# Kernel optimization log

Hardware: AMD Instinct MI355X
Metric: run time of the kernel (lower is better)

The kernel has to match this reference:

```python
import jax, jax.numpy as jnp
import numpy as np

B, F, V, D_EMB = 16384, 32, 50000, 16
D_IN = F * D_EMB            # 512, concat embedding dim
N_TASK, N_SPEC, N_SH = 2, 2, 2
E = N_TASK * N_SPEC + N_SH  # 6 experts per CGC level
H1, H2 = 512, 256           # expert_params dims
T1, T2 = 128, 64            # tower dims


def setup_inputs() -> dict:
    key = jax.random.key(0)
    ks = iter(jax.random.split(key, 32))
    def w(shape, s=0.05):
        return jax.random.normal(next(ks), shape, jnp.float32) * s
    return dict(
        x_ids=jax.random.randint(next(ks), (B, F), 0, V),
        emb=w((F, V, D_EMB)),
        e1_W1=w((E, D_IN, H1)), e1_b1=jnp.zeros((E, H1), jnp.float32),
        e1_W2=w((E, H1, H2)), e1_b2=jnp.zeros((E, H2), jnp.float32),
        g1_Ws=w((N_TASK, D_IN, N_SPEC + N_SH)), g1_bs=jnp.zeros((N_TASK, N_SPEC + N_SH), jnp.float32),
        g1_Wsh=w((D_IN, E)), g1_bsh=jnp.zeros((E,), jnp.float32),
        e2_W1=w((E, H2, H1)), e2_b1=jnp.zeros((E, H1), jnp.float32),
        e2_W2=w((E, H1, H2)), e2_b2=jnp.zeros((E, H2), jnp.float32),
        g2_Ws=w((N_TASK, H2, N_SPEC + N_SH)), g2_bs=jnp.zeros((N_TASK, N_SPEC + N_SH), jnp.float32),
        tw_W1=w((N_TASK, H2, T1)), tw_b1=jnp.zeros((N_TASK, T1), jnp.float32),
        tw_W2=w((N_TASK, T1, T2)), tw_b2=jnp.zeros((N_TASK, T2), jnp.float32),
    )


def _cgc(x_list, W1, b1, W2, b2, Wg, bg, Wg_sh=None, bg_sh=None):
    # Stack expert inputs: task-t specific experts read x_list[t], shared read x_list[-1].
    X = jnp.stack([x_list[0]] * N_SPEC + [x_list[1]] * N_SPEC + [x_list[-1]] * N_SH)  # [E,B,Din]
    # Grouped two-layer expert MLP (BatchNorm is identity at eval-mode init).
    h = jax.nn.relu(jnp.einsum('ebd,edh->ebh', X, W1) + b1[:, None, :])   # [E,B,H1]
    out = jax.nn.relu(jnp.einsum('ebh,eho->ebo', h, W2) + b2[:, None, :])  # [E,B,H2]
    outs = []
    for t in range(N_TASK):
        gate = jax.nn.softmax(x_list[t] @ Wg[t] + bg[t], axis=-1)          # [B, N_SPEC+N_SH]
        sel = jnp.concatenate([out[t * N_SPEC:(t + 1) * N_SPEC], out[-N_SH:]], axis=0)
        outs.append(jnp.einsum('bk,kbo->bo', gate, sel))
    if Wg_sh is not None:  # shared gate only for levels < n_level
        gate = jax.nn.softmax(x_list[-1] @ Wg_sh + bg_sh, axis=-1)          # [B,E]
        outs.append(jnp.einsum('bk,kbo->bo', gate, out))
    return outs


def reference(x_ids, emb, e1_W1, e1_b1, e1_W2, e1_b2, g1_Ws, g1_bs, g1_Wsh, g1_bsh,
              e2_W1, e2_b1, e2_W2, e2_b2, g2_Ws, g2_bs, tw_W1, tw_b1, tw_W2, tw_b2):
    # Embedding lookup per sparse feature, then flatten (squeeze_dim=True).
    embed_x = emb[jnp.arange(F)[None, :], x_ids].reshape(B, D_IN)  # [B, 512]
    xs = [embed_x] * (N_TASK + 1)
    xs = _cgc(xs, e1_W1, e1_b1, e1_W2, e1_b2, g1_Ws, g1_bs, g1_Wsh, g1_bsh)  # level 1 -> 3 outs
    xs = _cgc(xs, e2_W1, e2_b1, e2_W2, e2_b2, g2_Ws, g2_bs)                  # level 2 -> 2 outs
    ys = []
    for t in range(N_TASK):
        h = jax.nn.relu(xs[t] @ tw_W1[t] + tw_b1[t])
        h = jax.nn.relu(h @ tw_W2[t] + tw_b2[t])
        ys.append(jax.nn.sigmoid(h))  # PredictionLayer('classification')
    return jnp.concatenate(ys, axis=1)  # [B, N_TASK*T2]
```

## Files before the change

kernel.cpp:

```cpp
#include <hip/hip_runtime.h>

typedef unsigned short u16;
typedef __attribute__((ext_vector_type(4))) unsigned short u16x4;
typedef __attribute__((ext_vector_type(8))) unsigned short u16x8;
typedef __attribute__((ext_vector_type(8))) short s16x8;
typedef __attribute__((ext_vector_type(4))) float f32x4;

#define BATCH 16384
#define NFEAT 32
#define NVOCAB 50000

__device__ __forceinline__ u16 f2bf(float f) {
    union { float f; unsigned u; } v; v.f = f;
    unsigned u = v.u;
    return (u16)((u + 0x7fffu + ((u >> 16) & 1u)) >> 16);
}
__device__ __forceinline__ float bf2f(u16 h) {
    union { unsigned u; float f; } v; v.u = ((unsigned)h) << 16;
    return v.f;
}

__device__ __forceinline__ void load_lds16(const u16* g, u16* l) {
    __builtin_amdgcn_global_load_lds(
        (const __attribute__((address_space(1))) void*)g,
        (__attribute__((address_space(3))) void*)l, 16, 0, 0);
}

struct PrepDesc { const float* src; u16* dst; int K; int N; int nz; int zbase; };
struct PrepArgs { PrepDesc d[6]; };

__global__ void prep_weights(PrepArgs args) {
    int z = blockIdx.z;
    int di = 0;
    #pragma unroll
    for (int i = 0; i < 6; i++)
        if (z >= args.d[i].zbase && z < args.d[i].zbase + args.d[i].nz) di = i;
    PrepDesc d = args.d[di];
    int zz = z - d.zbase;
    int k0 = blockIdx.x * 32, n0 = blockIdx.y * 32;
    if (k0 >= d.K || n0 >= d.N) return;
    __shared__ float tile[32][33];
    const float* src = d.src + (long)zz * d.K * d.N;
    u16* dst = d.dst + (long)zz * d.K * d.N;
    int tx = threadIdx.x & 31, ty = threadIdx.x >> 5;
    for (int r = ty; r < 32; r += 8) {
        int k = k0 + r, n = n0 + tx;
        tile[r][tx] = (k < d.K && n < d.N) ? src[(long)k * d.N + n] : 0.f;
    }
    __syncthreads();
    for (int r = ty; r < 32; r += 8) {
        int n = n0 + r, k = k0 + tx;
        if (n < d.N && k < d.K) dst[(long)n * d.K + k] = f2bf(tile[tx][r]);
    }
}

__global__ void gather_embed(const int* __restrict__ ids,
                             const float* __restrict__ emb,
                             u16* __restrict__ out) {
    int idx = blockIdx.x * 256 + threadIdx.x;
    int d4 = idx & 3;
    int f  = (idx >> 2) & 31;
    int b  = idx >> 7;
    int id = ids[b * NFEAT + f];
    const float4* p = (const float4*)(emb + ((long)f * NVOCAB + id) * 16) + d4;
    float4 v = *p;
    u16x4 o;
    o.x = f2bf(v.x); o.y = f2bf(v.y); o.z = f2bf(v.z); o.w = f2bf(v.w);
    *(u16x4*)(out + (long)b * 512 + f * 16 + d4 * 4) = o;
}

struct GemmP {
    const u16* A; const u16* Bt; const float* bias; u16* C;
    int N, K, a_zshift, c_row_stride; long a_zstride, c_zstride;
};

__device__ __forceinline__ void gemm_impl(const GemmP p) {
    __shared__ u16 sA[128 * 64];
    __shared__ u16 sB[256 * 64];
    const int z = blockIdx.z;
    const u16* Ab = p.A + (long)(z >> p.a_zshift) * p.a_zstride;
    const u16* Bb = p.Bt + (long)z * p.N * p.K;
    const int m0 = blockIdx.x * 128;
    const int n0 = blockIdx.y * 256;
    const int tid = threadIdx.x;
    const int lane = tid & 63;
    const int w = tid >> 6;
    const int wm = (w & 1) * 64;
    const int wn = (w >> 1) * 128;
    const int l16 = lane & 15;
    const int q = lane >> 4;
    const int key = l16 & 7;
    const int K = p.K;

    const int tr = tid >> 3;
    const int lc = (tid & 7) ^ (tr & 7);
    const u16* gA0 = Ab + (long)(m0 + tr) * K + lc * 8;
    const u16* gB0 = Bb + (long)(n0 + tr) * K + lc * 8;
    u16* lA0 = &sA[(tid & ~63) * 8];
    u16* lB0 = &sB[(tid & ~63) * 8];

    f32x4 acc[4][8] = {};

    for (int k0 = 0; k0 < K; k0 += 64) {
        if (k0) __syncthreads();
        #pragma unroll
        for (int i = 0; i < 4; i++)
            load_lds16(gA0 + (long)(32 * i) * K + k0, lA0 + i * 256 * 8);
        #pragma unroll
        for (int i = 0; i < 8; i++)
            load_lds16(gB0 + (long)(32 * i) * K + k0, lB0 + i * 256 * 8);
        __syncthreads();
        #pragma unroll
        for (int kk = 0; kk < 2; kk++) {
            const int pc = ((kk << 2) | q) ^ key;
            s16x8 af[4], bf[8];
            #pragma unroll
            for (int mt = 0; mt < 4; mt++)
                af[mt] = *(const s16x8*)(&sA[(wm + mt * 16 + l16) * 64 + pc * 8]);
            #pragma unroll
            for (int nt = 0; nt < 8; nt++)
                bf[nt] = *(const s16x8*)(&sB[(wn + nt * 16 + l16) * 64 + pc * 8]);
            #pragma unroll
            for (int mt = 0; mt < 4; mt++)
                #pragma unroll
                for (int nt = 0; nt < 8; nt++)
                    acc[mt][nt] = __builtin_amdgcn_mfma_f32_16x16x32_bf16(
                        bf[nt], af[mt], acc[mt][nt], 0, 0, 0);
        }
    }

    const float* bb = p.bias + (long)z * p.N;
    u16* Cp = p.C + (long)z * p.c_zstride;
    #pragma unroll
    for (int mt = 0; mt < 4; mt++) {
        int grow = m0 + wm + mt * 16 + l16;
        u16* rowp = Cp + (long)grow * p.c_row_stride;
        #pragma unroll
        for (int nt = 0; nt < 8; nt++) {
            int gc = n0 + wn + nt * 16 + q * 4;
            float4 bv = *(const float4*)(bb + gc);
            f32x4 v = acc[mt][nt];
            v.x = fmaxf(v.x + bv.x, 0.f);
            v.y = fmaxf(v.y + bv.y, 0.f);
            v.z = fmaxf(v.z + bv.z, 0.f);
            v.w = fmaxf(v.w + bv.w, 0.f);
            u16x4 o;
            o.x = f2bf(v.x); o.y = f2bf(v.y); o.z = f2bf(v.z); o.w = f2bf(v.w);
            *(u16x4*)(rowp + gc) = o;
        }
    }
}

__global__ __launch_bounds__(256, 2) void gemm_l1a(GemmP p) { gemm_impl(p); }
__global__ __launch_bounds__(256, 2) void gemm_l1b(GemmP p) { gemm_impl(p); }
__global__ __launch_bounds__(256, 2) void gemm_l2a(GemmP p) { gemm_impl(p); }
__global__ __launch_bounds__(256, 2) void gemm_l2b(GemmP p) { gemm_impl(p); }

__global__ __launch_bounds__(256, 1)
void tower_fused(const u16* __restrict__ x2, const u16* __restrict__ W1t,
                 const float* __restrict__ b1, const u16* __restrict__ W2t,
                 const float* __restrict__ b2, float* __restrict__ out) {
    const int t = blockIdx.y, m0 = blockIdx.x * 64;
    __shared__ u16 sX[64 * 256];
    __shared__ u16 sW1[128 * 256];
    __shared__ u16 sH[64 * 136];
    __shared__ u16 sW2[64 * 128];
    __shared__ float sB1[128];
    __shared__ float sB2[64];
    const int tid = threadIdx.x, lane = tid & 63, w = tid >> 6;
    const int l16 = lane & 15, q = lane >> 4;

    #pragma unroll
    for (int i = 0; i < 8; i++) {
        int c = i * 256 + tid, row = c >> 5, kc = c & 31;
        int lcc = (kc & ~7) | ((kc & 7) ^ (row & 7));
        load_lds16(x2 + ((long)t * BATCH + m0 + row) * 256 + lcc * 8,
                   &sX[(i * 256 + (tid & ~63)) * 8]);
    }
    #pragma unroll
    for (int i = 0; i < 16; i++) {
        int c = i * 256 + tid, row = c >> 5, kc = c & 31;
        int lcc = (kc & ~7) | ((kc & 7) ^ (row & 7));
        load_lds16(W1t + ((long)t * 128 + row) * 256 + lcc * 8,
                   &sW1[(i * 256 + (tid & ~63)) * 8]);
    }
    #pragma unroll
    for (int i = 0; i < 4; i++) {
        int c = i * 256 + tid, row = c >> 4, kc = c & 15;
        int lcc = (kc & ~7) | ((kc & 7) ^ (row & 7));
        load_lds16(W2t + ((long)t * 64 + row) * 128 + lcc * 8,
                   &sW2[(i * 256 + (tid & ~63)) * 8]);
    }
    if (tid < 128) sB1[tid] = b1[t * 128 + tid];
    if (tid < 64)  sB2[tid] = b2[t * 64 + tid];
    __syncthreads();

    f32x4 acc1[4][2] = {};
    #pragma unroll
    for (int kk = 0; kk < 8; kk++) {
        int pcb = kk * 4 + q;
        s16x8 af[4], bf[2];
        #pragma unroll
        for (int mt = 0; mt < 4; mt++) {
            int row = mt * 16 + l16;
            int sc = (pcb & ~7) | ((pcb & 7) ^ (row & 7));
            af[mt] = *(const s16x8*)(&sX[row * 256 + sc * 8]);
        }
        #pragma unroll
        for (int nt = 0; nt < 2; nt++) {
            int row = w * 32 + nt * 16 + l16;
            int sc = (pcb & ~7) | ((pcb & 7) ^ (row & 7));
            bf[nt] = *(const s16x8*)(&sW1[row * 256 + sc * 8]);
        }
        #pragma unroll
        for (int mt = 0; mt < 4; mt++)
            #pragma unroll
            for (int nt = 0; nt < 2; nt++)
                acc1[mt][nt] = __builtin_amdgcn_mfma_f32_16x16x32_bf16(
                    bf[nt], af[mt], acc1[mt][nt], 0, 0, 0);
    }
    #pragma unroll
    for (int mt = 0; mt < 4; mt++) {
        int row = mt * 16 + l16;
        #pragma unroll
        for (int nt = 0; nt < 2; nt++) {
            int col = w * 32 + nt * 16 + q * 4;
            f32x4 v = acc1[mt][nt];
            u16x4 o;
            o.x = f2bf(fmaxf(v.x + sB1[col + 0], 0.f));
            o.y = f2bf(fmaxf(v.y + sB1[col + 1], 0.f));
            o.z = f2bf(fmaxf(v.z + sB1[col + 2], 0.f));
            o.w = f2bf(fmaxf(v.w + sB1[col + 3], 0.f));
            *(u16x4*)(&sH[row * 136 + col]) = o;
        }
    }
    __syncthreads();

    f32x4 acc2[4] = {};
    #pragma unroll
    for (int kk = 0; kk < 4; kk++) {
        s16x8 af[4], bf;
        #pragma unroll
        for (int mt = 0; mt < 4; mt++) {
            int row = mt * 16 + l16;
            af[mt] = *(const s16x8*)(&sH[row * 136 + kk * 32 + q * 8]);
        }
        {
            int row = w * 16 + l16;
            int pc = kk * 4 + q;
            int sc = (pc & ~7) | ((pc & 7) ^ (row & 7));
            bf = *(const s16x8*)(&sW2[row * 128 + sc * 8]);
        }
        #pragma unroll
        for (int mt = 0; mt < 4; mt++)
            acc2[mt] = __builtin_amdgcn_mfma_f32_16x16x32_bf16(
                bf, af[mt], acc2[mt], 0, 0, 0);
    }
    #pragma unroll
    for (int mt = 0; mt < 4; mt++) {
        int grow = m0 + mt * 16 + l16;
        int col = w * 16 + q * 4;
        float4 bv = *(const float4*)(sB2 + col);
        f32x4 v = acc2[mt];
        float4 r;
        r.x = 1.f / (1.f + __expf(-(v.x + bv.x)));
        r.y = 1.f / (1.f + __expf(-(v.y + bv.y)));
        r.z = 1.f / (1.f + __expf(-(v.z + bv.z)));
        r.w = 1.f / (1.f + __expf(-(v.w + bv.w)));
        *(float4*)(out + (long)grow * 128 + t * 64 + col) = r;
    }
}

__global__ __launch_bounds__(256)
void gate1(const u16* __restrict__ embed, const u16* __restrict__ out1,
           const float* __restrict__ g1Ws, const float* __restrict__ g1bs,
           const float* __restrict__ gWsh, const float* __restrict__ gbsh,
           u16* __restrict__ x1) {
    const int m0 = blockIdx.x * 8;
    __shared__ float sg[8][16];
    const int tid = threadIdx.x;
    const int row = tid >> 5, l = tid & 31;
    const long rb = m0 + row;

    float a[4] = {0,0,0,0}, b[4] = {0,0,0,0}, c[6] = {0,0,0,0,0,0};
    {
        const u16* er = embed + rb * 512 + l * 16;
        u16x8 xa = *(const u16x8*)(er);
        u16x8 xb = *(const u16x8*)(er + 8);
        #pragma unroll
        for (int u = 0; u < 16; u++) {
            int k = l * 16 + u;
            float xv = bf2f(u < 8 ? xa[u] : xb[u - 8]);
            float4 wa = *(const float4*)(g1Ws + k * 4);
            float4 wb = *(const float4*)(g1Ws + 2048 + k * 4);
            a[0] += xv * wa.x; a[1] += xv * wa.y; a[2] += xv * wa.z; a[3] += xv * wa.w;
            b[0] += xv * wb.x; b[1] += xv * wb.y; b[2] += xv * wb.z; b[3] += xv * wb.w;
            float2 w0 = *(const float2*)(gWsh + k * 6);
            float2 w1 = *(const float2*)(gWsh + k * 6 + 2);
            float2 w2 = *(const float2*)(gWsh + k * 6 + 4);
            c[0] += xv * w0.x; c[1] += xv * w0.y;
            c[2] += xv * w1.x; c[3] += xv * w1.y;
            c[4] += xv * w2.x; c[5] += xv * w2.y;
        }
    }
    #pragma unroll
    for (int off = 1; off < 32; off <<= 1) {
        #pragma unroll
        for (int g = 0; g < 4; g++) { a[g] += __shfl_xor(a[g], off); b[g] += __shfl_xor(b[g], off); }
        #pragma unroll
        for (int g = 0; g < 6; g++) c[g] += __shfl_xor(c[g], off);
    }
    if (l == 0) {
        float mx, s, e[6];
        mx = -1e30f;
        for (int g = 0; g < 4; g++) { a[g] += g1bs[g]; mx = fmaxf(mx, a[g]); }
        s = 0.f; for (int g = 0; g < 4; g++) { e[g] = __expf(a[g] - mx); s += e[g]; }
        for (int g = 0; g < 4; g++) sg[row][g] = e[g] / s;
        mx = -1e30f;
        for (int g = 0; g < 4; g++) { b[g] += g1bs[4 + g]; mx = fmaxf(mx, b[g]); }
        s = 0.f; for (int g = 0; g < 4; g++) { e[g] = __expf(b[g] - mx); s += e[g]; }
        for (int g = 0; g < 4; g++) sg[row][4 + g] = e[g] / s;
        mx = -1e30f;
        for (int g = 0; g < 6; g++) { c[g] += gbsh[g]; mx = fmaxf(mx, c[g]); }
        s = 0.f; for (int g = 0; g < 6; g++) { e[g] = __expf(c[g] - mx); s += e[g]; }
        for (int g = 0; g < 6; g++) sg[row][8 + g] = e[g] / s;
    }
    __syncthreads();

    const int c8 = l * 8;
    const u16* ob = out1 + rb * 256 + c8;
    u16x8 o[6];
    #pragma unroll
    for (int k = 0; k < 6; k++) o[k] = *(const u16x8*)(ob + (long)k * BATCH * 256);
    const float* g = sg[row];
    u16x8 r0, r1, r2;
    #pragma unroll
    for (int u = 0; u < 8; u++) {
        float o0 = bf2f(o[0][u]), o1 = bf2f(o[1][u]), o2 = bf2f(o[2][u]);
        float o3 = bf2f(o[3][u]), o4 = bf2f(o[4][u]), o5 = bf2f(o[5][u]);
        r0[u] = f2bf(g[0] * o0 + g[1] * o1 + g[2] * o4 + g[3] * o5);
        r1[u] = f2bf(g[4] * o2 + g[5] * o3 + g[6] * o4 + g[7] * o5);
        r2[u] = f2bf(g[8] * o0 + g[9] * o1 + g[10] * o2 + g[11] * o3 + g[12] * o4 + g[13] * o5);
    }
    *(u16x8*)(x1 + ((long)0 * BATCH + rb) * 256 + c8) = r0;
    *(u16x8*)(x1 + ((long)1 * BATCH + rb) * 256 + c8) = r1;
    *(u16x8*)(x1 + ((long)2 * BATCH + rb) * 256 + c8) = r2;
}

__global__ __launch_bounds__(256)
void gate2(const u16* __restrict__ x1, const u16* __restrict__ out2,
           const float* __restrict__ g2Ws, const float* __restrict__ g2bs,
           u16* __restrict__ x2) {
    const int m0 = blockIdx.x * 8;
    __shared__ float sg[8][8];
    const int tid = threadIdx.x;
    const int row = tid >> 5, l = tid & 31;
    const long rb = m0 + row;

    float a[4] = {0,0,0,0}, b[4] = {0,0,0,0};
    {
        const u16* e0 = x1 + rb * 256 + l * 8;
        const u16* e1 = e0 + (long)BATCH * 256;
        u16x8 x0 = *(const u16x8*)e0;
        u16x8 x1v = *(const u16x8*)e1;
        #pragma unroll
        for (int u = 0; u < 8; u++) {
            int k = l * 8 + u;
            float4 wa = *(const float4*)(g2Ws + k * 4);
            float4 wb = *(const float4*)(g2Ws + 1024 + k * 4);
            float xv0 = bf2f(x0[u]), xv1 = bf2f(x1v[u]);
            a[0] += xv0 * wa.x; a[1] += xv0 * wa.y; a[2] += xv0 * wa.z; a[3] += xv0 * wa.w;
            b[0] += xv1 * wb.x; b[1] += xv1 * wb.y; b[2] += xv1 * wb.z; b[3] += xv1 * wb.w;
        }
    }
    #pragma unroll
    for (int off = 1; off < 32; off <<= 1) {
        #pragma unroll
        for (int g = 0; g < 4; g++) { a[g] += __shfl_xor(a[g], off); b[g] += __shfl_xor(b[g], off); }
    }
    if (l == 0) {
        float mx, s, e[4];
        mx = -1e30f;
        for (int g = 0; g < 4; g++) { a[g] += g2bs[g]; mx = fmaxf(mx, a[g]); }
        s = 0.f; for (int g = 0; g < 4; g++) { e[g] = __expf(a[g] - mx); s += e[g]; }
        for (int g = 0; g < 4; g++) sg[row][g] = e[g] / s;
        mx = -1e30f;
        for (int g = 0; g < 4; g++) { b[g] += g2bs[4 + g]; mx = fmaxf(mx, b[g]); }
        s = 0.f; for (int g = 0; g < 4; g++) { e[g] = __expf(b[g] - mx); s += e[g]; }
        for (int g = 0; g < 4; g++) sg[row][4 + g] = e[g] / s;
    }
    __syncthreads();

    const int c8 = l * 8;
    const u16* ob = out2 + rb * 256 + c8;
    u16x8 o[6];
    #pragma unroll
    for (int k = 0; k < 6; k++) o[k] = *(const u16x8*)(ob + (long)k * BATCH * 256);
    const float* g = sg[row];
    u16x8 r0, r1;
    #pragma unroll
    for (int u = 0; u < 8; u++) {
        float o0 = bf2f(o[0][u]), o1 = bf2f(o[1][u]), o2 = bf2f(o[2][u]);
        float o3 = bf2f(o[3][u]), o4 = bf2f(o[4][u]), o5 = bf2f(o[5][u]);
        r0[u] = f2bf(g[0] * o0 + g[1] * o1 + g[2] * o4 + g[3] * o5);
        r1[u] = f2bf(g[4] * o2 + g[5] * o3 + g[6] * o4 + g[7] * o5);
    }
    *(u16x8*)(x2 + ((long)0 * BATCH + rb) * 256 + c8) = r0;
    *(u16x8*)(x2 + ((long)1 * BATCH + rb) * 256 + c8) = r1;
}

extern "C" void kernel_launch(void* const* d_in, const int* in_sizes, int n_in,
                              void* d_out, int out_size, void* d_ws, size_t ws_size,
                              hipStream_t stream) {
    const int*   x_ids = (const int*)  d_in[0];
    const float* emb   = (const float*)d_in[1];
    const float* e1W1  = (const float*)d_in[2];
    const float* e1b1  = (const float*)d_in[3];
    const float* e1W2  = (const float*)d_in[4];
    const float* e1b2  = (const float*)d_in[5];
    const float* g1Ws  = (const float*)d_in[6];
    const float* g1bs  = (const float*)d_in[7];
    const float* g1Wsh = (const float*)d_in[8];
    const float* g1bsh = (const float*)d_in[9];
    const float* e2W1  = (const float*)d_in[10];
    const float* e2b1  = (const float*)d_in[11];
    const float* e2W2  = (const float*)d_in[12];
    const float* e2b2  = (const float*)d_in[13];
    const float* g2Ws  = (const float*)d_in[14];
    const float* g2bs  = (const float*)d_in[15];
    const float* twW1  = (const float*)d_in[16];
    const float* twb1  = (const float*)d_in[17];
    const float* twW2  = (const float*)d_in[18];
    const float* twb2  = (const float*)d_in[19];
    float* out = (float*)d_out;

    char* ws = (char*)d_ws;
    u16* embed   = (u16*)(ws + 0);
    u16* wt_e1W1 = (u16*)(ws + 16777216);
    u16* wt_e1W2 = (u16*)(ws + 19922944);
    u16* wt_e2W1 = (u16*)(ws + 21495808);
    u16* wt_e2W2 = (u16*)(ws + 23068672);
    u16* wt_twW1 = (u16*)(ws + 24641536);
    u16* wt_twW2 = (u16*)(ws + 24772608);
    u16* h_buf   = (u16*)(ws + 24805376);
    u16* o_buf   = (u16*)(ws + 125468672);
    u16* x1      = (u16*)(ws + 175800320);
    u16* x2      = (u16*)(ws + 200966144);

    PrepArgs pa;
    pa.d[0] = { e1W1, wt_e1W1, 512, 512, 6,  0 };
    pa.d[1] = { e1W2, wt_e1W2, 512, 256, 6,  6 };
    pa.d[2] = { e2W1, wt_e2W1, 256, 512, 6, 12 };
    pa.d[3] = { e2W2, wt_e2W2, 512, 256, 6, 18 };
    pa.d[4] = { twW1, wt_twW1, 256, 128, 2, 24 };
    pa.d[5] = { twW2, wt_twW2, 128,  64, 2, 26 };
    prep_weights<<<dim3(16, 16, 28), 256, 0, stream>>>(pa);

    gather_embed<<<dim3(BATCH * NFEAT * 4 / 256), 256, 0, stream>>>(x_ids, emb, embed);

    GemmP p1a = { embed, wt_e1W1, e1b1, h_buf, 512, 512, 0, 512, 0L, (long)BATCH * 512 };
    gemm_l1a<<<dim3(128, 2, 6), 256, 0, stream>>>(p1a);

    GemmP p1b = { h_buf, wt_e1W2, e1b2, o_buf, 256, 512, 0, 256,
                  (long)BATCH * 512, (long)BATCH * 256 };
    gemm_l1b<<<dim3(128, 1, 6), 256, 0, stream>>>(p1b);

    gate1<<<dim3(BATCH / 8), 256, 0, stream>>>(embed, o_buf, g1Ws, g1bs, g1Wsh, g1bsh, x1);

    GemmP p2a = { x1, wt_e2W1, e2b1, h_buf, 512, 256, 1, 512,
                  (long)BATCH * 256, (long)BATCH * 512 };
    gemm_l2a<<<dim3(128, 2, 6), 256, 0, stream>>>(p2a);

    GemmP p2b = { h_buf, wt_e2W2, e2b2, o_buf, 256, 512, 0, 256,
                  (long)BATCH * 512, (long)BATCH * 256 };
    gemm_l2b<<<dim3(128, 1, 6), 256, 0, stream>>>(p2b);

    gate2<<<dim3(BATCH / 8), 256, 0, stream>>>(x1, o_buf, g2Ws, g2bs, x2);

    tower_fused<<<dim3(BATCH / 64, 2), 256, 0, stream>>>(x2, wt_twW1, twb1, wt_twW2, twb2, out);
}
```

Measured before the change: 522.7 us.

## Fuse level-2 gating into tower kernel and merge gather with weight prep

Combines embedding gather and weight transpose/convert into one persistent-style launch. Fuses the level-2 gate softmax and weighted expert mix directly into the tower MLP kernel, so the x2 intermediate is never written to or reread from global memory. Tower weights are now read straight from global/L2 instead of being staged in LDS, which lowers LDS use to allow two blocks per CU. The p1a a_zshift changes from 0 to 3, which only means all experts read the same embed input, the same as before since a_zstride is 0.

```diff
diff --git a/kernel.cpp b/kernel.cpp
--- a/kernel.cpp
+++ b/kernel.cpp
@@ -19,54 +19,65 @@
     union { unsigned u; float f; } v; v.u = ((unsigned)h) << 16;
     return v.f;
 }
-
 __device__ __forceinline__ void load_lds16(const u16* g, u16* l) {
     __builtin_amdgcn_global_load_lds(
         (const __attribute__((address_space(1))) void*)g,
         (__attribute__((address_space(3))) void*)l, 16, 0, 0);
 }
 
-struct PrepDesc { const float* src; u16* dst; int K; int N; int nz; int zbase; };
-struct PrepArgs { PrepDesc d[6]; };
-
-__global__ void prep_weights(PrepArgs args) {
-    int z = blockIdx.z;
-    int di = 0;
-    #pragma unroll
-    for (int i = 0; i < 6; i++)
-        if (z >= args.d[i].zbase && z < args.d[i].zbase + args.d[i].nz) di = i;
-    PrepDesc d = args.d[di];
-    int zz = z - d.zbase;
-    int k0 = blockIdx.x * 32, n0 = blockIdx.y * 32;
-    if (k0 >= d.K || n0 >= d.N) return;
-    __shared__ float tile[32][33];
-    const float* src = d.src + (long)zz * d.K * d.N;
-    u16* dst = d.dst + (long)zz * d.K * d.N;
-    int tx = threadIdx.x & 31, ty = threadIdx.x >> 5;
-    for (int r = ty; r < 32; r += 8) {
-        int k = k0 + r, n = n0 + tx;
-        tile[r][tx] = (k < d.K && n < d.N) ? src[(long)k * d.N + n] : 0.f;
-    }
-    __syncthreads();
-    for (int r = ty; r < 32; r += 8) {
-        int n = n0 + r, k = k0 + tx;
-        if (n < d.N && k < d.K) dst[(long)n * d.K + k] = f2bf(tile[tx][r]);
-    }
-}
-
-__global__ void gather_embed(const int* __restrict__ ids,
-                             const float* __restrict__ emb,
-                             u16* __restrict__ out) {
-    int idx = blockIdx.x * 256 + threadIdx.x;
-    int d4 = idx & 3;
-    int f  = (idx >> 2) & 31;
-    int b  = idx >> 7;
-    int id = ids[b * NFEAT + f];
-    const float4* p = (const float4*)(emb + ((long)f * NVOCAB + id) * 16) + d4;
-    float4 v = *p;
-    u16x4 o;
-    o.x = f2bf(v.x); o.y = f2bf(v.y); o.z = f2bf(v.z); o.w = f2bf(v.w);
-    *(u16x4*)(out + (long)b * 512 + f * 16 + d4 * 4) = o;
+struct P0Args {
+    const int* x_ids; const float* emb;
+    const float* e1W1; const float* e1W2; const float* e2W1; const float* e2W2;
+    const float* twW1; const float* twW2;
+    u16* embed; u16* wt_e1W1; u16* wt_e1W2; u16* wt_e2W1; u16* wt_e2W2;
+    u16* wt_twW1; u16* wt_twW2;
+};
+
+__global__ __launch_bounds__(256)
+void p0_gather_prep(P0Args a) {
+    __shared__ float tile[32 * 33];
+    const int tid = threadIdx.x;
+    if (blockIdx.x < 256) {
+        for (long idx = (long)blockIdx.x * 256 + tid; idx < (long)BATCH * NFEAT * 4;
+             idx += 65536) {
+            int d4 = (int)(idx & 3);
+            int f  = (int)((idx >> 2) & 31);
+            int b  = (int)(idx >> 7);
+            int id = a.x_ids[b * NFEAT + f];
+            float4 v = *((const float4*)(a.emb + ((long)f * NVOCAB + id) * 16) + d4);
+            u16x4 o;
+            o.x = f2bf(v.x); o.y = f2bf(v.y); o.z = f2bf(v.z); o.w = f2bf(v.w);
+            *(u16x4*)(a.embed + (long)b * 512 + f * 16 + d4 * 4) = o;
+        }
+    } else {
+        const int tx = tid & 31, ty = tid >> 5;
+        for (int j = blockIdx.x - 256; j < 7168; j += 256) {
+            int z = j >> 8;
+            int rem = j & 255;
+            const float* src; u16* dst; int K, N, zb;
+            if      (z <  6) { src = a.e1W1; dst = a.wt_e1W1; K = 512; N = 512; zb = 0; }
+            else if (z < 12) { src = a.e1W2; dst = a.wt_e1W2; K = 512; N = 256; zb = 6; }
+            else if (z < 18) { src = a.e2W1; dst = a.wt_e2W1; K = 256; N = 512; zb = 12; }
+            else if (z < 24) { src = a.e2W2; dst = a.wt_e2W2; K = 512; N = 256; zb = 18; }
+            else if (z < 26) { src = a.twW1; dst = a.wt_twW1; K = 256; N = 128; zb = 24; }
+            else             { src = a.twW2; dst = a.wt_twW2; K = 128; N = 64;  zb = 26; }
+            int zz = z - zb;
+            int k0 = (rem & 15) * 32, n0 = (rem >> 4) * 32;
+            if (k0 >= K || n0 >= N) continue;
+            __syncthreads();
+            const float* s = src + (long)zz * K * N;
+            u16* d = dst + (long)zz * K * N;
+            for (int r = ty; r < 32; r += 8) {
+                int k = k0 + r, n = n0 + tx;
+                tile[r * 33 + tx] = (k < K && n < N) ? s[(long)k * N + n] : 0.f;
+            }
+            __syncthreads();
+            for (int r = ty; r < 32; r += 8) {
+                int n = n0 + r, k = k0 + tx;
+                if (n < N && k < K) d[(long)n * K + k] = f2bf(tile[tx * 33 + r]);
+            }
+        }
+    }
 }
 
 struct GemmP {
@@ -156,121 +167,6 @@
 __global__ __launch_bounds__(256, 2) void gemm_l2a(GemmP p) { gemm_impl(p); }
 __global__ __launch_bounds__(256, 2) void gemm_l2b(GemmP p) { gemm_impl(p); }
 
-__global__ __launch_bounds__(256, 1)
-void tower_fused(const u16* __restrict__ x2, const u16* __restrict__ W1t,
-                 const float* __restrict__ b1, const u16* __restrict__ W2t,
-                 const float* __restrict__ b2, float* __restrict__ out) {
-    const int t = blockIdx.y, m0 = blockIdx.x * 64;
-    __shared__ u16 sX[64 * 256];
-    __shared__ u16 sW1[128 * 256];
-    __shared__ u16 sH[64 * 136];
-    __shared__ u16 sW2[64 * 128];
-    __shared__ float sB1[128];
-    __shared__ float sB2[64];
-    const int tid = threadIdx.x, lane = tid & 63, w = tid >> 6;
-    const int l16 = lane & 15, q = lane >> 4;
-
-    #pragma unroll
-    for (int i = 0; i < 8; i++) {
-        int c = i * 256 + tid, row = c >> 5, kc = c & 31;
-        int lcc = (kc & ~7) | ((kc & 7) ^ (row & 7));
-        load_lds16(x2 + ((long)t * BATCH + m0 + row) * 256 + lcc * 8,
-                   &sX[(i * 256 + (tid & ~63)) * 8]);
-    }
-    #pragma unroll
-    for (int i = 0; i < 16; i++) {
-        int c = i * 256 + tid, row = c >> 5, kc = c & 31;
-        int lcc = (kc & ~7) | ((kc & 7) ^ (row & 7));
-        load_lds16(W1t + ((long)t * 128 + row) * 256 + lcc * 8,
-                   &sW1[(i * 256 + (tid & ~63)) * 8]);
-    }
-    #pragma unroll
-    for (int i = 0; i < 4; i++) {
-        int c = i * 256 + tid, row = c >> 4, kc = c & 15;
-        int lcc = (kc & ~7) | ((kc & 7) ^ (row & 7));
-        load_lds16(W2t + ((long)t * 64 + row) * 128 + lcc * 8,
-                   &sW2[(i * 256 + (tid & ~63)) * 8]);
-    }
-    if (tid < 128) sB1[tid] = b1[t * 128 + tid];
-    if (tid < 64)  sB2[tid] = b2[t * 64 + tid];
-    __syncthreads();
-
-    f32x4 acc1[4][2] = {};
-    #pragma unroll
-    for (int kk = 0; kk < 8; kk++) {
-        int pcb = kk * 4 + q;
-        s16x8 af[4], bf[2];
-        #pragma unroll
-        for (int mt = 0; mt < 4; mt++) {
-            int row = mt * 16 + l16;
-            int sc = (pcb & ~7) | ((pcb & 7) ^ (row & 7));
-            af[mt] = *(const s16x8*)(&sX[row * 256 + sc * 8]);
-        }
-        #pragma unroll
-        for (int nt = 0; nt < 2; nt++) {
-            int row = w * 32 + nt * 16 + l16;
-            int sc = (pcb & ~7) | ((pcb & 7) ^ (row & 7));
-            bf[nt] = *(const s16x8*)(&sW1[row * 256 + sc * 8]);
-        }
-        #pragma unroll
-        for (int mt = 0; mt < 4; mt++)
-            #pragma unroll
-            for (int nt = 0; nt < 2; nt++)
-                acc1[mt][nt] = __builtin_amdgcn_mfma_f32_16x16x32_bf16(
-                    bf[nt], af[mt], acc1[mt][nt], 0, 0, 0);
-    }
-    #pragma unroll
-    for (int mt = 0; mt < 4; mt++) {
-        int row = mt * 16 + l16;
-        #pragma unroll
-        for (int nt = 0; nt < 2; nt++) {
-            int col = w * 32 + nt * 16 + q * 4;
-            f32x4 v = acc1[mt][nt];
-            u16x4 o;
-            o.x = f2bf(fmaxf(v.x + sB1[col + 0], 0.f));
-            o.y = f2bf(fmaxf(v.y + sB1[col + 1], 0.f));
-            o.z = f2bf(fmaxf(v.z + sB1[col + 2], 0.f));
-            o.w = f2bf(fmaxf(v.w + sB1[col + 3], 0.f));
-            *(u16x4*)(&sH[row * 136 + col]) = o;
-        }
-    }
-    __syncthreads();
-
-    f32x4 acc2[4] = {};
-    #pragma unroll
-    for (int kk = 0; kk < 4; kk++) {
-        s16x8 af[4], bf;
-        #pragma unroll
-        for (int mt = 0; mt < 4; mt++) {
-            int row = mt * 16 + l16;
-            af[mt] = *(const s16x8*)(&sH[row * 136 + kk * 32 + q * 8]);
-        }
-        {
-            int row = w * 16 + l16;
-            int pc = kk * 4 + q;
-            int sc = (pc & ~7) | ((pc & 7) ^ (row & 7));
-            bf = *(const s16x8*)(&sW2[row * 128 + sc * 8]);
-        }
-        #pragma unroll
-        for (int mt = 0; mt < 4; mt++)
-            acc2[mt] = __builtin_amdgcn_mfma_f32_16x16x32_bf16(
-                bf, af[mt], acc2[mt], 0, 0, 0);
-    }
-    #pragma unroll
-    for (int mt = 0; mt < 4; mt++) {
-        int grow = m0 + mt * 16 + l16;
-        int col = w * 16 + q * 4;
-        float4 bv = *(const float4*)(sB2 + col);
-        f32x4 v = acc2[mt];
-        float4 r;
-        r.x = 1.f / (1.f + __expf(-(v.x + bv.x)));
-        r.y = 1.f / (1.f + __expf(-(v.y + bv.y)));
-        r.z = 1.f / (1.f + __expf(-(v.z + bv.z)));
-        r.w = 1.f / (1.f + __expf(-(v.w + bv.w)));
-        *(float4*)(out + (long)grow * 128 + t * 64 + col) = r;
-    }
-}
-
 __global__ __launch_bounds__(256)
 void gate1(const u16* __restrict__ embed, const u16* __restrict__ out1,
            const float* __restrict__ g1Ws, const float* __restrict__ g1bs,
@@ -347,66 +243,149 @@
     *(u16x8*)(x1 + ((long)2 * BATCH + rb) * 256 + c8) = r2;
 }
 
-__global__ __launch_bounds__(256)
-void gate2(const u16* __restrict__ x1, const u16* __restrict__ out2,
-           const float* __restrict__ g2Ws, const float* __restrict__ g2bs,
-           u16* __restrict__ x2) {
-    const int m0 = blockIdx.x * 8;
-    __shared__ float sg[8][8];
-    const int tid = threadIdx.x;
-    const int row = tid >> 5, l = tid & 31;
-    const long rb = m0 + row;
-
-    float a[4] = {0,0,0,0}, b[4] = {0,0,0,0};
+__global__ __launch_bounds__(256, 2)
+void tower_g2(const u16* __restrict__ x1, const u16* __restrict__ out2,
+              const float* __restrict__ g2Ws, const float* __restrict__ g2bs,
+              const u16* __restrict__ twW1t, const float* __restrict__ twb1,
+              const u16* __restrict__ twW2t, const float* __restrict__ twb2,
+              float* __restrict__ out) {
+    const int t = blockIdx.y, m0 = blockIdx.x * 64;
+    __shared__ u16 sX[64 * 256];
+    __shared__ u16 sH[64 * 128];
+    __shared__ float sg[64][4];
+    const int tid = threadIdx.x, lane = tid & 63, w4 = tid >> 6;
+    const int l16 = lane & 15, q = lane >> 4;
+
+    const int row = tid >> 2, p = tid & 3;
     {
-        const u16* e0 = x1 + rb * 256 + l * 8;
-        const u16* e1 = e0 + (long)BATCH * 256;
-        u16x8 x0 = *(const u16x8*)e0;
-        u16x8 x1v = *(const u16x8*)e1;
-        #pragma unroll
-        for (int u = 0; u < 8; u++) {
-            int k = l * 8 + u;
-            float4 wa = *(const float4*)(g2Ws + k * 4);
-            float4 wb = *(const float4*)(g2Ws + 1024 + k * 4);
-            float xv0 = bf2f(x0[u]), xv1 = bf2f(x1v[u]);
-            a[0] += xv0 * wa.x; a[1] += xv0 * wa.y; a[2] += xv0 * wa.z; a[3] += xv0 * wa.w;
-            b[0] += xv1 * wb.x; b[1] += xv1 * wb.y; b[2] += xv1 * wb.z; b[3] += xv1 * wb.w;
-        }
-    }
-    #pragma unroll
-    for (int off = 1; off < 32; off <<= 1) {
-        #pragma unroll
-        for (int g = 0; g < 4; g++) { a[g] += __shfl_xor(a[g], off); b[g] += __shfl_xor(b[g], off); }
-    }
-    if (l == 0) {
-        float mx, s, e[4];
-        mx = -1e30f;
-        for (int g = 0; g < 4; g++) { a[g] += g2bs[g]; mx = fmaxf(mx, a[g]); }
-        s = 0.f; for (int g = 0; g < 4; g++) { e[g] = __expf(a[g] - mx); s += e[g]; }
-        for (int g = 0; g < 4; g++) sg[row][g] = e[g] / s;
-        mx = -1e30f;
-        for (int g = 0; g < 4; g++) { b[g] += g2bs[4 + g]; mx = fmaxf(mx, b[g]); }
-        s = 0.f; for (int g = 0; g < 4; g++) { e[g] = __expf(b[g] - mx); s += e[g]; }
-        for (int g = 0; g < 4; g++) sg[row][4 + g] = e[g] / s;
+        const u16* xr = x1 + ((long)t * BATCH + m0 + row) * 256 + p * 64;
+        const float* W = g2Ws + t * 1024;
+        float a[4] = {0, 0, 0, 0};
+        #pragma unroll
+        for (int j = 0; j < 8; j++) {
+            u16x8 xv8 = *(const u16x8*)(xr + j * 8);
+            #pragma unroll
+            for (int u = 0; u < 8; u++) {
+                int k = p * 64 + j * 8 + u;
+                float4 wv = *(const float4*)(W + k * 4);
+                float xv = bf2f(xv8[u]);
+                a[0] += xv * wv.x; a[1] += xv * wv.y; a[2] += xv * wv.z; a[3] += xv * wv.w;
+            }
+        }
+        #pragma unroll
+        for (int g = 0; g < 4; g++) { a[g] += __shfl_xor(a[g], 1); a[g] += __shfl_xor(a[g], 2); }
+        if (p == 0) {
+            float mx = -1e30f, s = 0.f, e[4];
+            for (int g = 0; g < 4; g++) { a[g] += g2bs[t * 4 + g]; mx = fmaxf(mx, a[g]); }
+            for (int g = 0; g < 4; g++) { e[g] = __expf(a[g] - mx); s += e[g]; }
+            for (int g = 0; g < 4; g++) sg[row][g] = e[g] / s;
+        }
     }
     __syncthreads();
 
-    const int c8 = l * 8;
-    const u16* ob = out2 + rb * 256 + c8;
-    u16x8 o[6];
-    #pragma unroll
-    for (int k = 0; k < 6; k++) o[k] = *(const u16x8*)(ob + (long)k * BATCH * 256);
-    const float* g = sg[row];
-    u16x8 r0, r1;
-    #pragma unroll
-    for (int u = 0; u < 8; u++) {
-        float o0 = bf2f(o[0][u]), o1 = bf2f(o[1][u]), o2 = bf2f(o[2][u]);
-        float o3 = bf2f(o[3][u]), o4 = bf2f(o[4][u]), o5 = bf2f(o[5][u]);
-        r0[u] = f2bf(g[0] * o0 + g[1] * o1 + g[2] * o4 + g[3] * o5);
-        r1[u] = f2bf(g[4] * o2 + g[5] * o3 + g[6] * o4 + g[7] * o5);
-    }
-    *(u16x8*)(x2 + ((long)0 * BATCH + rb) * 256 + c8) = r0;
-    *(u16x8*)(x2 + ((long)1 * BATCH + rb) * 256 + c8) = r1;
+    {
+        const long rb = m0 + row;
+        const float* g = sg[row];
+        const u16* o0p = out2 + ((long)(2 * t)     * BATCH + rb) * 256 + p * 64;
+        const u16* o1p = out2 + ((long)(2 * t + 1) * BATCH + rb) * 256 + p * 64;
+        const u16* o4p = out2 + ((long)4           * BATCH + rb) * 256 + p * 64;
+        const u16* o5p = out2 + ((long)5           * BATCH + rb) * 256 + p * 64;
+        #pragma unroll
+        for (int j = 0; j < 8; j++) {
+            u16x8 v0 = *(const u16x8*)(o0p + j * 8);
+            u16x8 v1 = *(const u16x8*)(o1p + j * 8);
+            u16x8 v4 = *(const u16x8*)(o4p + j * 8);
+            u16x8 v5 = *(const u16x8*)(o5p + j * 8);
+            u16x8 r;
+            #pragma unroll
+            for (int u = 0; u < 8; u++)
+                r[u] = f2bf(g[0] * bf2f(v0[u]) + g[1] * bf2f(v1[u]) +
+                            g[2] * bf2f(v4[u]) + g[3] * bf2f(v5[u]));
+            int c = p * 8 + j;
+            int pc = (c & ~7) | ((c & 7) ^ (row & 7));
+            *(u16x8*)(&sX[row * 256 + pc * 8]) = r;
+        }
+    }
+    __syncthreads();
+
+    const u16* W1 = twW1t + (long)t * 128 * 256;
+    const u16* W2 = twW2t + (long)t * 64 * 128;
+    f32x4 acc1[4][2] = {};
+    #pragma unroll
+    for (int kk = 0; kk < 8; kk++) {
+        s16x8 af[4], bf[2];
+        #pragma unroll
+        for (int nt = 0; nt < 2; nt++) {
+            int nrow = w4 * 32 + nt * 16 + l16;
+            bf[nt] = *(const s16x8*)(W1 + (long)nrow * 256 + kk * 32 + q * 8);
+        }
+        #pragma unroll
+        for (int mt = 0; mt < 4; mt++) {
+            int rrow = mt * 16 + l16;
+            int cc = kk * 4 + q;
+            int pc = (cc & ~7) | ((cc & 7) ^ (rrow & 7));
+            af[mt] = *(const s16x8*)(&sX[rrow * 256 + pc * 8]);
+        }
+        #pragma unroll
+        for (int mt = 0; mt < 4; mt++)
+            #pragma unroll
+            for (int nt = 0; nt < 2; nt++)
+                acc1[mt][nt] = __builtin_amdgcn_mfma_f32_16x16x32_bf16(
+                    bf[nt], af[mt], acc1[mt][nt], 0, 0, 0);
+    }
+    #pragma unroll
+    for (int mt = 0; mt < 4; mt++) {
+        int rrow = mt * 16 + l16;
+        #pragma unroll
+        for (int nt = 0; nt < 2; nt++) {
+            int col = w4 * 32 + nt * 16 + q * 4;
+            float4 bv = *(const float4*)(twb1 + t * 128 + col);
+            f32x4 v = acc1[mt][nt];
+            u16x4 o;
+            o.x = f2bf(fmaxf(v.x + bv.x, 0.f));
+            o.y = f2bf(fmaxf(v.y + bv.y, 0.f));
+            o.z = f2bf(fmaxf(v.z + bv.z, 0.f));
+            o.w = f2bf(fmaxf(v.w + bv.w, 0.f));
+            int c = col >> 3;
+            int pc = (c & ~7) | ((c & 7) ^ (rrow & 7));
+            *(u16x4*)(&sH[rrow * 128 + pc * 8 + (col & 7)]) = o;
+        }
+    }
+    __syncthreads();
+
+    f32x4 acc2[4] = {};
+    #pragma unroll
+    for (int kk = 0; kk < 4; kk++) {
+        s16x8 af[4], bfv;
+        {
+            int nrow = w4 * 16 + l16;
+            bfv = *(const s16x8*)(W2 + (long)nrow * 128 + kk * 32 + q * 8);
+        }
+        #pragma unroll
+        for (int mt = 0; mt < 4; mt++) {
+            int rrow = mt * 16 + l16;
+            int cc = kk * 4 + q;
+            int pc = (cc & ~7) | ((cc & 7) ^ (rrow & 7));
+            af[mt] = *(const s16x8*)(&sH[rrow * 128 + pc * 8]);
+        }
+        #pragma unroll
+        for (int mt = 0; mt < 4; mt++)
+            acc2[mt] = __builtin_amdgcn_mfma_f32_16x16x32_bf16(
+                bfv, af[mt], acc2[mt], 0, 0, 0);
+    }
+    #pragma unroll
+    for (int mt = 0; mt < 4; mt++) {
+        int grow = m0 + mt * 16 + l16;
+        int col = w4 * 16 + q * 4;
+        float4 bv = *(const float4*)(twb2 + t * 64 + col);
+        f32x4 v = acc2[mt];
+        float4 r;
+        r.x = 1.f / (1.f + __expf(-(v.x + bv.x)));
+        r.y = 1.f / (1.f + __expf(-(v.y + bv.y)));
+        r.z = 1.f / (1.f + __expf(-(v.z + bv.z)));
+        r.w = 1.f / (1.f + __expf(-(v.w + bv.w)));
+        *(float4*)(out + (long)grow * 128 + t * 64 + col) = r;
+    }
 }
 
 extern "C" void kernel_launch(void* const* d_in, const int* in_sizes, int n_in,
@@ -445,20 +424,17 @@
     u16* h_buf   = (u16*)(ws + 24805376);
     u16* o_buf   = (u16*)(ws + 125468672);
     u16* x1      = (u16*)(ws + 175800320);
-    u16* x2      = (u16*)(ws + 200966144);
-
-    PrepArgs pa;
-    pa.d[0] = { e1W1, wt_e1W1, 512, 512, 6,  0 };
-    pa.d[1] = { e1W2, wt_e1W2, 512, 256, 6,  6 };
-    pa.d[2] = { e2W1, wt_e2W1, 256, 512, 6, 12 };
-    pa.d[3] = { e2W2, wt_e2W2, 512, 256, 6, 18 };
-    pa.d[4] = { twW1, wt_twW1, 256, 128, 2, 24 };
-    pa.d[5] = { twW2, wt_twW2, 128,  64, 2, 26 };
-    prep_weights<<<dim3(16, 16, 28), 256, 0, stream>>>(pa);
-
-    gather_embed<<<dim3(BATCH * NFEAT * 4 / 256), 256, 0, stream>>>(x_ids, emb, embed);
-
-    GemmP p1a = { embed, wt_e1W1, e1b1, h_buf, 512, 512, 0, 512, 0L, (long)BATCH * 512 };
+
+    P0Args p0;
+    p0.x_ids = x_ids; p0.emb = emb;
+    p0.e1W1 = e1W1; p0.e1W2 = e1W2; p0.e2W1 = e2W1; p0.e2W2 = e2W2;
+    p0.twW1 = twW1; p0.twW2 = twW2;
+    p0.embed = embed; p0.wt_e1W1 = wt_e1W1; p0.wt_e1W2 = wt_e1W2;
+    p0.wt_e2W1 = wt_e2W1; p0.wt_e2W2 = wt_e2W2;
+    p0.wt_twW1 = wt_twW1; p0.wt_twW2 = wt_twW2;
+    p0_gather_prep<<<dim3(512), 256, 0, stream>>>(p0);
+
+    GemmP p1a = { embed, wt_e1W1, e1b1, h_buf, 512, 512, 3, 512, 0L, (long)BATCH * 512 };
     gemm_l1a<<<dim3(128, 2, 6), 256, 0, stream>>>(p1a);
 
     GemmP p1b = { h_buf, wt_e1W2, e1b2, o_buf, 256, 512, 0, 256,
@@ -475,7 +451,6 @@
                   (long)BATCH * 512, (long)BATCH * 256 };
     gemm_l2b<<<dim3(128, 1, 6), 256, 0, stream>>>(p2b);
 
-    gate2<<<dim3(BATCH / 8), 256, 0, stream>>>(x1, o_buf, g2Ws, g2bs, x2);
-
-    tower_fused<<<dim3(BATCH / 64, 2), 256, 0, stream>>>(x2, wt_twW1, twb1, wt_twW2, twb2, out);
-}
+    tower_g2<<<dim3(BATCH / 64, 2), 256, 0, stream>>>(
+        x1, o_buf, g2Ws, g2bs, wt_twW1, twb1, wt_twW2, twb2, out);
+}
```

Result: slower. 557.5 us (+6.7%).
